# Kernel tuning notes

Hardware: AMD Instinct MI355X
Metric: run time of the kernel (lower is better)

Reference implementation:

```python
import jax, jax.numpy as jnp
import numpy as np

EPS_AGG = 1e-6  # torch code adds 1e-6 to scatter weight sums
EPS_BN = 1e-5


def _pix_idx(loc_orig, H, W):
    # map normalized coords in [-1,1] to flat pixel index on an HxW grid
    loc = jnp.clip(loc_orig, -1.0, 1.0) * 0.5 + 0.5
    ix = jnp.round(loc[..., 0] * (W - 1)).astype(jnp.int32)
    iy = jnp.round(loc[..., 1] * (H - 1)).astype(jnp.int32)
    return iy * W + ix  # [B, N0]


def token2map(x, loc_orig, idx_agg, H, W):
    # scatter token features to a dense map, averaging collisions
    B, N, C = x.shape
    N0 = idx_agg.shape[1]
    idx_hw = _pix_idx(loc_orig, H, W)                                   # [B, N0]
    tok = jnp.take_along_axis(x, idx_agg[..., None], axis=1)            # [B, N0, C]
    flat = (idx_hw + jnp.arange(B, dtype=jnp.int32)[:, None] * (H * W)).reshape(-1)
    sums = jax.ops.segment_sum(tok.reshape(-1, C), flat, num_segments=B * H * W)
    cnt = jax.ops.segment_sum(jnp.ones((B * N0,), x.dtype), flat, num_segments=B * H * W)
    out = sums / (cnt[:, None] + EPS_AGG)
    return out.reshape(B, H, W, C).transpose(0, 3, 1, 2)                # [B, C, H, W]


def map2token(fmap, Nt, loc_orig, idx_agg_t, agg_weight_t):
    # gather map pixels back to Nt target tokens, weighted-averaging per token
    B, C, H, W = fmap.shape
    idx_hw = _pix_idx(loc_orig, H, W)                                   # [B, N0]
    pix = fmap.transpose(0, 2, 3, 1).reshape(B, H * W, C)
    gath = jnp.take_along_axis(pix, idx_hw[..., None], axis=1)          # [B, N0, C]
    flat = (idx_agg_t + jnp.arange(B, dtype=jnp.int32)[:, None] * Nt).reshape(-1)
    num = jax.ops.segment_sum((gath * agg_weight_t[..., None]).reshape(-1, C), flat, num_segments=B * Nt)
    den = jax.ops.segment_sum(agg_weight_t.reshape(-1), flat, num_segments=B * Nt)
    return (num / (den[:, None] + EPS_AGG)).reshape(B, Nt, C)


def token_downup(x, idx_agg_s, idx_agg_t, agg_weight_t, Nt):
    # weighted aggregation from N source tokens to Nt target tokens via N0 original positions
    B, N, C = x.shape
    src = jnp.take_along_axis(x, idx_agg_s[..., None], axis=1)          # [B, N0, C]
    flat = (idx_agg_t + jnp.arange(B, dtype=jnp.int32)[:, None] * Nt).reshape(-1)
    num = jax.ops.segment_sum((src * agg_weight_t[..., None]).reshape(-1, C), flat, num_segments=B * Nt)
    den = jax.ops.segment_sum(agg_weight_t.reshape(-1), flat, num_segments=B * Nt)
    return (num / (den[:, None] + EPS_AGG)).reshape(B, Nt, C)


def batchnorm(x, gamma, beta):
    # BatchNorm2d on [B,C,Nt,1] == per-channel stats over (B, Nt); x here is [B, Nt, C]
    mu = x.mean(axis=(0, 1), keepdims=True)
    var = x.var(axis=(0, 1), keepdims=True)
    return (x - mu) * jax.lax.rsqrt(var + EPS_BN) * gamma + beta


def setup_inputs() -> dict:
    key = jax.random.key(0)
    ks = jax.random.split(key, 12)
    B, N, N0, Nt, Cin, Cout, H, W = 32, 1568, 3136, 784, 256, 512, 56, 56
    x = jax.random.normal(ks[0], (B, N, Cin), dtype=jnp.float32)
    loc_orig = jax.random.uniform(ks[1], (B, N0, 2), dtype=jnp.float32, minval=-1.0, maxval=1.0)
    idx_agg = jax.random.randint(ks[2], (B, N0), 0, N, dtype=jnp.int32)
    agg_weight = jax.random.uniform(ks[3], (B, N0), dtype=jnp.float32)
    idx_agg_t = jax.random.randint(ks[4], (B, N0), 0, Nt, dtype=jnp.int32)
    agg_weight_t = jax.random.uniform(ks[5], (B, N0), dtype=jnp.float32)
    dw_w = jax.random.normal(ks[6], (Cin, 1, 3, 3), dtype=jnp.float32) * 0.1     # depthwise 3x3
    skip_w = jax.random.normal(ks[7], (Cin,), dtype=jnp.float32) * 0.1           # depthwise 1x1
    conv_w = jax.random.normal(ks[8], (Cout, Cin), dtype=jnp.float32) * (1.0 / np.sqrt(Cin))
    gamma1 = jnp.ones((Cin,), jnp.float32); beta1 = jnp.zeros((Cin,), jnp.float32)
    gamma2 = jnp.ones((Cout,), jnp.float32); beta2 = jnp.zeros((Cout,), jnp.float32)
    return {"x": x, "loc_orig": loc_orig, "idx_agg": idx_agg, "agg_weight": agg_weight,
            "idx_agg_t": idx_agg_t, "agg_weight_t": agg_weight_t, "H": H, "W": W, "Nt": Nt,
            "dw_w": dw_w, "skip_w": skip_w, "conv_w": conv_w,
            "gamma1": gamma1, "beta1": beta1, "gamma2": gamma2, "beta2": beta2}


def reference(x, loc_orig, idx_agg, agg_weight, idx_agg_t, agg_weight_t, H, W, Nt,
              dw_w, skip_w, conv_w, gamma1, beta1, gamma2, beta2):
    # token -> map scatter
    x_map = token2map(x, loc_orig, idx_agg, H, W)                       # [B, Cin, H, W]
    # 3x3 depthwise conv, stride 2, padding 1
    Cin = x_map.shape[1]
    x_map = jax.lax.conv_general_dilated(
        x_map, dw_w, window_strides=(2, 2), padding=((1, 1), (1, 1)),
        feature_group_count=Cin, dimension_numbers=("NCHW", "OIHW", "NCHW"))    # [B, Cin, H/2, W/2]
    # map -> target tokens gather
    x_back = map2token(x_map, Nt, loc_orig, idx_agg_t, agg_weight_t)    # [B, Nt, Cin]
    # skip path: token downsample + 1x1 depthwise (per-channel scale)
    xs = token_downup(x, idx_agg, idx_agg_t, agg_weight_t, Nt)          # [B, Nt, Cin]
    xs = xs * skip_w                                                    # dw_skip, groups=Cin, k=1
    y = xs + x_back
    y = batchnorm(y, gamma1, beta1)
    y = jnp.einsum("bnc,oc->bno", y, conv_w)                            # 1x1 conv Cin->Cout
    y = batchnorm(y, gamma2, beta2)
    return jax.nn.relu(y)                                               # [B, Nt, Cout]
```

## Files before the change

kernel.cpp:

```cpp
#include <hip/hip_runtime.h>

constexpr int B    = 32;
constexpr int N    = 1568;
constexpr int N0   = 3136;
constexpr int Nt   = 784;
constexpr int Cin  = 256;
constexpr int Cout = 512;
constexpr int H    = 56;
constexpr int W    = 56;
constexpr int HW   = 3136;
constexpr int Ho   = 28;
constexpr int Wo   = 28;
constexpr int HWo  = 784;
constexpr int RR   = B * Nt;
constexpr int NE   = B * N0;
constexpr int NBP  = B * HW;
constexpr int NBT  = B * Nt;
constexpr int NB   = NBP + NBT;
constexpr int NCHUNK = NB / 256;

constexpr size_t W_HIST  = 0;
constexpr size_t W_S1SUM = NB;
constexpr size_t W_S1SQ  = W_S1SUM + Cin;
constexpr size_t W_S2SUM = W_S1SQ + Cin;
constexpr size_t W_S2SQ  = W_S2SUM + Cout;
constexpr size_t W_OFF   = NB + 1536;
constexpr size_t W_CUR   = W_OFF + NB + 8;
constexpr size_t W_P56   = W_CUR + NB;
constexpr size_t W_P28   = W_P56 + NE;
constexpr size_t W_BSUM  = W_P28 + NE;
constexpr size_t W_SRTS  = W_BSUM + 512;
constexpr size_t W_STS   = W_SRTS + NE;
constexpr size_t W_STP   = W_STS + NE;
constexpr size_t W_STW   = W_STP + NE;
constexpr size_t W_CONVB = W_STW + NE;
constexpr size_t W_YBF   = W_CONVB + (size_t)B * HWo * Cin / 2;
constexpr size_t W_WFB   = W_YBF + (size_t)RR * Cin / 2;
constexpr size_t W_BIAS  = W_WFB + (size_t)Cout * Cin / 2;
constexpr size_t W_A2    = W_BIAS + Cout;
constexpr size_t W_C2    = W_A2 + Cout;
constexpr size_t W_ZB    = W_C2 + Cout;

__device__ __forceinline__ int pix_of(float t, float scale) {
    t = fminf(fmaxf(t, -1.0f), 1.0f);
    float u = __fadd_rn(__fmul_rn(t, 0.5f), 0.5f);
    return (int)rintf(__fmul_rn(u, scale));
}
__device__ __forceinline__ unsigned short f2bf(float f) {
    unsigned int u = __float_as_uint(f);
    u = (u + 0x7fffu + ((u >> 16) & 1u)) >> 16;
    return (unsigned short)u;
}
__device__ __forceinline__ float bf2f(unsigned short h) {
    return __uint_as_float(((unsigned int)h) << 16);
}

__global__ void k_hist(const float* __restrict__ loc, const int* __restrict__ idxt,
                       int* __restrict__ hist, int* __restrict__ p56a, int* __restrict__ p28a) {
    int i = blockIdx.x * 256 + threadIdx.x;
    if (i >= NE) return;
    int b = i / N0;
    float lx = loc[(size_t)2 * i], ly = loc[(size_t)2 * i + 1];
    int p56 = pix_of(ly, 55.0f) * W + pix_of(lx, 55.0f);
    int p28 = pix_of(ly, 27.0f) * Wo + pix_of(lx, 27.0f);
    p56a[i] = p56; p28a[i] = p28;
    atomicAdd(&hist[b * HW + p56], 1);
    atomicAdd(&hist[NBP + b * Nt + idxt[i]], 1);
}

__global__ void k_scanA(const int* __restrict__ hist, int* __restrict__ bsum) {
    __shared__ int sm[256];
    int i = blockIdx.x * 256 + threadIdx.x;
    sm[threadIdx.x] = hist[i];
    __syncthreads();
    for (int d = 128; d > 0; d >>= 1) {
        if (threadIdx.x < d) sm[threadIdx.x] += sm[threadIdx.x + d];
        __syncthreads();
    }
    if (threadIdx.x == 0) bsum[blockIdx.x] = sm[0];
}

__global__ void k_scanB(int* __restrict__ bsum) {
    __shared__ int sm[512];
    int t = threadIdx.x;
    int v = (t < NCHUNK) ? bsum[t] : 0;
    sm[t] = v; __syncthreads();
    for (int d = 1; d < 512; d <<= 1) {
        int u = (t >= d) ? sm[t - d] : 0;
        __syncthreads();
        sm[t] += u;
        __syncthreads();
    }
    if (t < NCHUNK) bsum[t] = sm[t] - v;
}

__global__ void k_scanC(const int* __restrict__ hist, const int* __restrict__ bsum,
                        int* __restrict__ off, int* __restrict__ cur) {
    __shared__ int sm[256];
    int t = threadIdx.x;
    int i = blockIdx.x * 256 + t;
    int v = hist[i];
    sm[t] = v; __syncthreads();
    for (int d = 1; d < 256; d <<= 1) {
        int u = (t >= d) ? sm[t - d] : 0;
        __syncthreads();
        sm[t] += u;
        __syncthreads();
    }
    int excl = bsum[blockIdx.x] + sm[t] - v;
    off[i] = excl; cur[i] = excl;
    if (i == NB - 1) off[NB] = excl + v;
}

__global__ void k_scatteridx(const int* __restrict__ p56a, const int* __restrict__ p28a,
                             const int* __restrict__ idxa, const int* __restrict__ idxt,
                             const float* __restrict__ wt, int* __restrict__ cur,
                             int* __restrict__ srtS, int* __restrict__ sTs,
                             int* __restrict__ sTp, float* __restrict__ sTw) {
    int i = blockIdx.x * 256 + threadIdx.x;
    if (i >= NE) return;
    int b = i / N0;
    int s = idxa[i];
    int posP = atomicAdd(&cur[b * HW + p56a[i]], 1);
    srtS[posP] = s;
    int posT = atomicAdd(&cur[NBP + b * Nt + idxt[i]], 1) - NE;
    sTs[posT] = s; sTp[posT] = p28a[i]; sTw[posT] = wt[i];
}

constexpr int GCAP = 512;
__global__ __launch_bounds__(256) void k_gconv(const float* __restrict__ x,
        const int* __restrict__ off, const int* __restrict__ srtS,
        const float* __restrict__ dww, unsigned short* __restrict__ convb) {
    __shared__ int   sPk[GCAP];
    __shared__ float sRc[GCAP];
    __shared__ int sSt[9], sCt[9], sPref[10];
    int blk = blockIdx.x;
    int c   = threadIdx.x;
    int b   = blk / HWo;
    int rem = blk - b * HWo;
    int oy  = rem / Wo;
    int ox  = rem - oy * Wo;
    if (c < 9) {
        int ky = c / 3, kx = c - ky * 3;
        int iy = oy * 2 - 1 + ky, ix = ox * 2 - 1 + kx;
        int st = 0, ct = 0;
        if (iy >= 0 && iy < H && ix >= 0 && ix < W) {
            int bin = b * HW + iy * W + ix;
            st = off[bin];
            ct = off[bin + 1] - st;
        }
        sSt[c] = st; sCt[c] = ct;
    }
    __syncthreads();
    if (c == 0) {
        int a = 0;
#pragma unroll
        for (int k = 0; k < 9; ++k) { sPref[k] = a; a += sCt[k]; }
        sPref[9] = a;
    }
    __syncthreads();
    int T = sPref[9];
    float wv[9];
#pragma unroll
    for (int k = 0; k < 9; ++k) wv[k] = dww[c * 9 + k];
    float acc = 0.0f;
    for (int base = 0; base < T; base += GCAP) {
        if (c < 9) {
            int ct = sCt[c], pr = sPref[c], st = sSt[c];
            float rc = 1.0f / ((float)ct + 1e-6f);
            int j0 = max(base - pr, 0);
            int j1 = min(base + GCAP - pr, ct);
            for (int j = j0; j < j1; ++j) {
                sPk[pr + j - base] = srtS[st + j] | (c << 16);
                sRc[pr + j - base] = rc;
            }
        }
        __syncthreads();
        int cnt = min(T - base, GCAP);
        for (int j = 0; j < cnt; ++j) {
            int pk = sPk[j];
            float rc = sRc[j];
            int s = pk & 0xFFFF, tap = pk >> 16;
            acc = fmaf(x[((size_t)b * N + s) * Cin + c] * rc, wv[tap], acc);
        }
        __syncthreads();
    }
    convb[(size_t)blk * Cin + c] = f2bf(acc);
}

constexpr int TCAP = 256;
__global__ __launch_bounds__(256) void k_gtok(const float* __restrict__ x,
        const unsigned short* __restrict__ convb, const int* __restrict__ off,
        const int* __restrict__ sTs, const int* __restrict__ sTp,
        const float* __restrict__ sTw, const float* __restrict__ skipw,
        unsigned short* __restrict__ ybf) {
    __shared__ int sS[TCAP];
    __shared__ int sP[TCAP];
    __shared__ float sW[TCAP];
    int bt = blockIdx.x;
    int c  = threadIdx.x;
    int b  = bt / Nt;
    int st = off[NBP + bt] - NE, en = off[NBP + bt + 1] - NE;
    int T = en - st;
    float sk = skipw[c];
    float acc = 0.0f, wsum = 0.0f;
    for (int base = 0; base < T; base += TCAP) {
        int cnt = min(T - base, TCAP);
        if (c < cnt) {
            sS[c] = sTs[st + base + c];
            sP[c] = sTp[st + base + c];
            sW[c] = sTw[st + base + c];
        }
        __syncthreads();
        for (int j = 0; j < cnt; ++j) {
            int s = sS[j], p = sP[j];
            float w = sW[j];
            wsum += w;
            float cv = bf2f(convb[((size_t)b * HWo + p) * Cin + c]);
            acc = fmaf(w, cv + sk * x[((size_t)b * N + s) * Cin + c], acc);
        }
        __syncthreads();
    }
    ybf[(size_t)bt * Cin + c] = f2bf(acc * (1.0f / (wsum + 1e-6f)));
}

__global__ void k_ystats(const unsigned short* __restrict__ ybf,
                         float* __restrict__ s1, float* __restrict__ s1q) {
    int c = threadIdx.x;
    float sum = 0.0f, sq = 0.0f;
    for (int r = blockIdx.x; r < RR; r += gridDim.x) {
        float v = bf2f(ybf[(size_t)r * Cin + c]);
        sum += v;
        sq = fmaf(v, v, sq);
    }
    atomicAdd(&s1[c], sum);
    atomicAdd(&s1q[c], sq);
}

__global__ void k_fold(const float* __restrict__ s1, const float* __restrict__ s1q,
                       const float* __restrict__ g1, const float* __restrict__ b1,
                       const float* __restrict__ convw, unsigned short* __restrict__ wfb,
                       float* __restrict__ bias) {
    int o = blockIdx.x, c = threadIdx.x;
    const float inv = 1.0f / (float)RR;
    float mu  = s1[c] * inv;
    float var = s1q[c] * inv - mu * mu;
    float a   = g1[c] / sqrtf(var + 1e-5f);
    float bs  = b1[c] - mu * a;
    float wv  = convw[(size_t)o * Cin + c];
    wfb[(size_t)o * Cin + c] = f2bf(wv * a);
    __shared__ float red[256];
    red[c] = wv * bs;
    __syncthreads();
    for (int st = 128; st > 0; st >>= 1) {
        if (c < st) red[c] += red[c + st];
        __syncthreads();
    }
    if (c == 0) bias[o] = red[0];
}

typedef __attribute__((ext_vector_type(8))) short short8;
typedef __attribute__((ext_vector_type(4))) float f32x4;

__global__ __launch_bounds__(256) void k_gemm(const unsigned short* __restrict__ A,
        const unsigned short* __restrict__ Bt, const float* __restrict__ bias,
        unsigned short* __restrict__ zb, float* __restrict__ s2, float* __restrict__ s2q) {
    constexpr int BK = 32, LS = 48;
    __shared__ unsigned short As[128 * LS];
    __shared__ unsigned short Bs[128 * LS];
    __shared__ float rsum[128], rsq[128];
    int m0 = blockIdx.x * 128, n0 = blockIdx.y * 128;
    int t = threadIdx.x;
    int wave = t >> 6, lane = t & 63;
    int wm = wave >> 1, wn = wave & 1;
    int l16 = lane & 15, lq = lane >> 4;
    f32x4 acc[4][4];
#pragma unroll
    for (int i = 0; i < 4; ++i)
#pragma unroll
        for (int j = 0; j < 4; ++j) acc[i][j] = (f32x4)0.0f;
    if (t < 128) { rsum[t] = 0.0f; rsq[t] = 0.0f; }

    for (int k0 = 0; k0 < Cin; k0 += BK) {
#pragma unroll
        for (int r2 = 0; r2 < 2; ++r2) {
            int e = r2 * 256 + t;
            int row = e >> 2, kc = (e & 3) * 8;
            *(float4*)&As[row * LS + kc] = *(const float4*)&A[((size_t)(m0 + row)) * Cin + k0 + kc];
            *(float4*)&Bs[row * LS + kc] = *(const float4*)&Bt[((size_t)(n0 + row)) * Cin + k0 + kc];
        }
        __syncthreads();
        short8 af[4], bf[4];
#pragma unroll
        for (int i = 0; i < 4; ++i) {
            af[i] = *(short8*)&As[(wm * 64 + i * 16 + l16) * LS + lq * 8];
            bf[i] = *(short8*)&Bs[(wn * 64 + i * 16 + l16) * LS + lq * 8];
        }
#pragma unroll
        for (int i = 0; i < 4; ++i)
#pragma unroll
            for (int j = 0; j < 4; ++j)
                acc[i][j] = __builtin_amdgcn_mfma_f32_16x16x32_bf16(af[i], bf[j], acc[i][j], 0, 0, 0);
        __syncthreads();
    }
#pragma unroll
    for (int j = 0; j < 4; ++j) {
        int cl  = wn * 64 + j * 16 + l16;
        int col = n0 + cl;
        float bv = bias[col];
        float ps = 0.0f, pq = 0.0f;
#pragma unroll
        for (int i = 0; i < 4; ++i) {
            int rbase = m0 + wm * 64 + i * 16 + lq * 4;
#pragma unroll
            for (int r = 0; r < 4; ++r) {
                float v = acc[i][j][r] + bv;
                zb[(size_t)(rbase + r) * Cout + col] = f2bf(v);
                ps += v;
                pq = fmaf(v, v, pq);
            }
        }
        atomicAdd(&rsum[cl], ps);
        atomicAdd(&rsq[cl], pq);
    }
    __syncthreads();
    if (t < 128) {
        atomicAdd(&s2[n0 + t], rsum[t]);
        atomicAdd(&s2q[n0 + t], rsq[t]);
    }
}

__global__ void k_fold2(const float* __restrict__ s2, const float* __restrict__ s2q,
                        const float* __restrict__ g2, const float* __restrict__ b2,
                        float* __restrict__ a2, float* __restrict__ c2) {
    int o = threadIdx.x;
    const float inv = 1.0f / (float)RR;
    float mu  = s2[o] * inv;
    float var = s2q[o] * inv - mu * mu;
    float a   = g2[o] / sqrtf(var + 1e-5f);
    a2[o] = a;
    c2[o] = b2[o] - mu * a;
}

__global__ void k_final(const unsigned short* __restrict__ zb, const float* __restrict__ a2,
                        const float* __restrict__ c2, float* __restrict__ out) {
    size_t j4 = ((size_t)blockIdx.x * 256 + threadIdx.x) * 4;
    int o = (int)(j4 & (Cout - 1));
    uint2 u = *(const uint2*)&zb[j4];
    float e0 = bf2f((unsigned short)(u.x & 0xffffu));
    float e1 = bf2f((unsigned short)(u.x >> 16));
    float e2 = bf2f((unsigned short)(u.y & 0xffffu));
    float e3 = bf2f((unsigned short)(u.y >> 16));
    float4 r;
    r.x = fmaxf(fmaf(e0, a2[o + 0], c2[o + 0]), 0.0f);
    r.y = fmaxf(fmaf(e1, a2[o + 1], c2[o + 1]), 0.0f);
    r.z = fmaxf(fmaf(e2, a2[o + 2], c2[o + 2]), 0.0f);
    r.w = fmaxf(fmaf(e3, a2[o + 3], c2[o + 3]), 0.0f);
    *(float4*)&out[j4] = r;
}

extern "C" void kernel_launch(void* const* d_in, const int* in_sizes, int n_in,
                              void* d_out, int out_size, void* d_ws, size_t ws_size,
                              hipStream_t stream) {
    const float* x     = (const float*)d_in[0];
    const float* loc   = (const float*)d_in[1];
    const int*   idxa  = (const int*)d_in[2];
    const int*   idxt  = (const int*)d_in[4];
    const float* wt    = (const float*)d_in[5];
    const float* dww   = (const float*)d_in[9];
    const float* skipw = (const float*)d_in[10];
    const float* convw = (const float*)d_in[11];
    const float* g1    = (const float*)d_in[12];
    const float* b1    = (const float*)d_in[13];
    const float* g2    = (const float*)d_in[14];
    const float* b2    = (const float*)d_in[15];

    float* ws = (float*)d_ws;
    int*   hist  = (int*)(ws + W_HIST);
    float* s1sum = ws + W_S1SUM;
    float* s1sq  = ws + W_S1SQ;
    float* s2sum = ws + W_S2SUM;
    float* s2sq  = ws + W_S2SQ;
    int*   off   = (int*)(ws + W_OFF);
    int*   cur   = (int*)(ws + W_CUR);
    int*   p56a  = (int*)(ws + W_P56);
    int*   p28a  = (int*)(ws + W_P28);
    int*   bsum  = (int*)(ws + W_BSUM);
    int*   srtS  = (int*)(ws + W_SRTS);
    int*   sTs   = (int*)(ws + W_STS);
    int*   sTp   = (int*)(ws + W_STP);
    float* sTw   = ws + W_STW;
    unsigned short* convb = (unsigned short*)(ws + W_CONVB);
    unsigned short* ybf   = (unsigned short*)(ws + W_YBF);
    unsigned short* wfb   = (unsigned short*)(ws + W_WFB);
    float* bias  = ws + W_BIAS;
    float* a2    = ws + W_A2;
    float* c2    = ws + W_C2;
    unsigned short* zb = (unsigned short*)(ws + W_ZB);
    float* out   = (float*)d_out;

    hipMemsetAsync(hist, 0, (size_t)(NB + 1536) * sizeof(float), stream);

    k_hist<<<NE / 256, 256, 0, stream>>>(loc, idxt, hist, p56a, p28a);
    k_scanA<<<NCHUNK, 256, 0, stream>>>(hist, bsum);
    k_scanB<<<1, 512, 0, stream>>>(bsum);
    k_scanC<<<NCHUNK, 256, 0, stream>>>(hist, bsum, off, cur);
    k_scatteridx<<<NE / 256, 256, 0, stream>>>(p56a, p28a, idxa, idxt, wt, cur, srtS, sTs, sTp, sTw);

    k_gconv<<<B * HWo, 256, 0, stream>>>(x, off, srtS, dww, convb);
    k_gtok<<<NBT, 256, 0, stream>>>(x, convb, off, sTs, sTp, sTw, skipw, ybf);
    k_ystats<<<256, 256, 0, stream>>>(ybf, s1sum, s1sq);
    k_fold<<<Cout, 256, 0, stream>>>(s1sum, s1sq, g1, b1, convw, wfb, bias);

    dim3 gg(RR / 128, Cout / 128);
    k_gemm<<<gg, 256, 0, stream>>>(ybf, wfb, bias, zb, s2sum, s2sq);
    k_fold2<<<1, 512, 0, stream>>>(s2sum, s2sq, g2, b2, a2, c2);
    k_final<<<(int)(((size_t)RR * Cout) / 1024), 256, 0, stream>>>(zb, a2, c2, out);
}
```

Baseline: 302.7 us.

## Bin source entries directly per conv output pixel with precomputed tap and weight

The binning stage now buckets each original position into every stride-2 conv output pixel whose 3x3 window covers it. Each entry stores the source token, tap index and reciprocal collision count, so k_gconv walks one contiguous list with no per-block 9-bin prefix gathering, shared staging or extra syncs. Token lists are packed into int2 entries and the gather loops are unrolled to keep several loads in flight. In exchange, k_hist and k_scat do up to four atomics and writes per entry, and the conv list is up to four times larger.

```diff
diff --git a/kernel.cpp b/kernel.cpp
--- a/kernel.cpp
+++ b/kernel.cpp
@@ -16,24 +16,23 @@
 constexpr int NE   = B * N0;
 constexpr int NBP  = B * HW;
 constexpr int NBT  = B * Nt;
-constexpr int NB   = NBP + NBT;
-constexpr int NCHUNK = NB / 256;
-
-constexpr size_t W_HIST  = 0;
-constexpr size_t W_S1SUM = NB;
+constexpr int NBO  = B * HWo;
+constexpr int SB   = NBT + NBO;
+constexpr int NCHUNK = SB / 256;
+
+constexpr size_t W_HISTP = 0;
+constexpr size_t W_HISTS = NBP;
+constexpr size_t W_S1SUM = NBP + SB;
 constexpr size_t W_S1SQ  = W_S1SUM + Cin;
 constexpr size_t W_S2SUM = W_S1SQ + Cin;
 constexpr size_t W_S2SQ  = W_S2SUM + Cout;
-constexpr size_t W_OFF   = NB + 1536;
-constexpr size_t W_CUR   = W_OFF + NB + 8;
-constexpr size_t W_P56   = W_CUR + NB;
-constexpr size_t W_P28   = W_P56 + NE;
-constexpr size_t W_BSUM  = W_P28 + NE;
-constexpr size_t W_SRTS  = W_BSUM + 512;
-constexpr size_t W_STS   = W_SRTS + NE;
-constexpr size_t W_STP   = W_STS + NE;
-constexpr size_t W_STW   = W_STP + NE;
-constexpr size_t W_CONVB = W_STW + NE;
+constexpr size_t W_OFF   = NBP + SB + 1536;
+constexpr size_t W_CUR   = W_OFF + SB + 8;
+constexpr size_t W_PC    = W_CUR + SB;
+constexpr size_t W_BSUM  = W_PC + NE;
+constexpr size_t W_LT    = W_BSUM + 512;
+constexpr size_t W_LC    = W_LT + (size_t)2 * NE;
+constexpr size_t W_CONVB = W_LC + (size_t)8 * NE;
 constexpr size_t W_YBF   = W_CONVB + (size_t)B * HWo * Cin / 2;
 constexpr size_t W_WFB   = W_YBF + (size_t)RR * Cin / 2;
 constexpr size_t W_BIAS  = W_WFB + (size_t)Cout * Cin / 2;
@@ -56,16 +55,23 @@
 }
 
 __global__ void k_hist(const float* __restrict__ loc, const int* __restrict__ idxt,
-                       int* __restrict__ hist, int* __restrict__ p56a, int* __restrict__ p28a) {
+                       int* __restrict__ histP, int* __restrict__ histS,
+                       int* __restrict__ pc) {
     int i = blockIdx.x * 256 + threadIdx.x;
     if (i >= NE) return;
     int b = i / N0;
     float lx = loc[(size_t)2 * i], ly = loc[(size_t)2 * i + 1];
-    int p56 = pix_of(ly, 55.0f) * W + pix_of(lx, 55.0f);
-    int p28 = pix_of(ly, 27.0f) * Wo + pix_of(lx, 27.0f);
-    p56a[i] = p56; p28a[i] = p28;
-    atomicAdd(&hist[b * HW + p56], 1);
-    atomicAdd(&hist[NBP + b * Nt + idxt[i]], 1);
+    int ix = pix_of(lx, 55.0f), iy = pix_of(ly, 55.0f);
+    int jx = pix_of(lx, 27.0f), jy = pix_of(ly, 27.0f);
+    int p56 = iy * W + ix, p28 = jy * Wo + jx;
+    pc[i] = p56 | (p28 << 16);
+    atomicAdd(&histP[b * HW + p56], 1);
+    atomicAdd(&histS[b * Nt + idxt[i]], 1);
+    int oy_lo = iy >> 1, oy_hi = min(Ho - 1, (iy + 1) >> 1);
+    int ox_lo = ix >> 1, ox_hi = min(Wo - 1, (ix + 1) >> 1);
+    for (int oy = oy_lo; oy <= oy_hi; ++oy)
+        for (int ox = ox_lo; ox <= ox_hi; ++ox)
+            atomicAdd(&histS[NBT + b * HWo + oy * Wo + ox], 1);
 }
 
 __global__ void k_scanA(const int* __restrict__ hist, int* __restrict__ bsum) {
@@ -109,117 +115,95 @@
     }
     int excl = bsum[blockIdx.x] + sm[t] - v;
     off[i] = excl; cur[i] = excl;
-    if (i == NB - 1) off[NB] = excl + v;
-}
-
-__global__ void k_scatteridx(const int* __restrict__ p56a, const int* __restrict__ p28a,
-                             const int* __restrict__ idxa, const int* __restrict__ idxt,
-                             const float* __restrict__ wt, int* __restrict__ cur,
-                             int* __restrict__ srtS, int* __restrict__ sTs,
-                             int* __restrict__ sTp, float* __restrict__ sTw) {
+    if (i == SB - 1) off[SB] = excl + v;
+}
+
+__global__ void k_scat(const int* __restrict__ pc, const int* __restrict__ idxa,
+                       const int* __restrict__ idxt, const float* __restrict__ wt,
+                       const int* __restrict__ histP, int* __restrict__ cur,
+                       int2* __restrict__ listT, int2* __restrict__ listC) {
     int i = blockIdx.x * 256 + threadIdx.x;
     if (i >= NE) return;
     int b = i / N0;
+    int v = pc[i];
+    int p56 = v & 0xFFFF, p28 = v >> 16;
     int s = idxa[i];
-    int posP = atomicAdd(&cur[b * HW + p56a[i]], 1);
-    srtS[posP] = s;
-    int posT = atomicAdd(&cur[NBP + b * Nt + idxt[i]], 1) - NE;
-    sTs[posT] = s; sTp[posT] = p28a[i]; sTw[posT] = wt[i];
-}
-
-constexpr int GCAP = 512;
+    int posT = atomicAdd(&cur[b * Nt + idxt[i]], 1);
+    listT[posT] = make_int2(s | (p28 << 16), __float_as_int(wt[i]));
+    float wrc = 1.0f / ((float)histP[b * HW + p56] + 1e-6f);
+    int wrci = __float_as_int(wrc);
+    int iy = p56 / W, ix = p56 - iy * W;
+    int oy_lo = iy >> 1, oy_hi = min(Ho - 1, (iy + 1) >> 1);
+    int ox_lo = ix >> 1, ox_hi = min(Wo - 1, (ix + 1) >> 1);
+    for (int oy = oy_lo; oy <= oy_hi; ++oy)
+        for (int ox = ox_lo; ox <= ox_hi; ++ox) {
+            int tap = (iy - (2 * oy - 1)) * 3 + (ix - (2 * ox - 1));
+            int posC = atomicAdd(&cur[NBT + b * HWo + oy * Wo + ox], 1) - NE;
+            listC[posC] = make_int2(s | (tap << 16), wrci);
+        }
+}
+
 __global__ __launch_bounds__(256) void k_gconv(const float* __restrict__ x,
-        const int* __restrict__ off, const int* __restrict__ srtS,
+        const int* __restrict__ off, const int2* __restrict__ listC,
         const float* __restrict__ dww, unsigned short* __restrict__ convb) {
-    __shared__ int   sPk[GCAP];
-    __shared__ float sRc[GCAP];
-    __shared__ int sSt[9], sCt[9], sPref[10];
-    int blk = blockIdx.x;
-    int c   = threadIdx.x;
-    int b   = blk / HWo;
-    int rem = blk - b * HWo;
-    int oy  = rem / Wo;
-    int ox  = rem - oy * Wo;
-    if (c < 9) {
-        int ky = c / 3, kx = c - ky * 3;
-        int iy = oy * 2 - 1 + ky, ix = ox * 2 - 1 + kx;
-        int st = 0, ct = 0;
-        if (iy >= 0 && iy < H && ix >= 0 && ix < W) {
-            int bin = b * HW + iy * W + ix;
-            st = off[bin];
-            ct = off[bin + 1] - st;
-        }
-        sSt[c] = st; sCt[c] = ct;
-    }
+    __shared__ float wsm[9 * 256];
+    int blk = blockIdx.x, c = threadIdx.x;
+    int b = blk / HWo;
+#pragma unroll
+    for (int k = 0; k < 9; ++k) wsm[k * 256 + c] = dww[c * 9 + k];
+    int st = off[NBT + blk] - NE, en = off[NBT + blk + 1] - NE;
     __syncthreads();
-    if (c == 0) {
-        int a = 0;
-#pragma unroll
-        for (int k = 0; k < 9; ++k) { sPref[k] = a; a += sCt[k]; }
-        sPref[9] = a;
-    }
-    __syncthreads();
-    int T = sPref[9];
-    float wv[9];
-#pragma unroll
-    for (int k = 0; k < 9; ++k) wv[k] = dww[c * 9 + k];
+    const float* xb = x + (size_t)b * N * Cin + c;
     float acc = 0.0f;
-    for (int base = 0; base < T; base += GCAP) {
-        if (c < 9) {
-            int ct = sCt[c], pr = sPref[c], st = sSt[c];
-            float rc = 1.0f / ((float)ct + 1e-6f);
-            int j0 = max(base - pr, 0);
-            int j1 = min(base + GCAP - pr, ct);
-            for (int j = j0; j < j1; ++j) {
-                sPk[pr + j - base] = srtS[st + j] | (c << 16);
-                sRc[pr + j - base] = rc;
-            }
-        }
-        __syncthreads();
-        int cnt = min(T - base, GCAP);
-        for (int j = 0; j < cnt; ++j) {
-            int pk = sPk[j];
-            float rc = sRc[j];
-            int s = pk & 0xFFFF, tap = pk >> 16;
-            acc = fmaf(x[((size_t)b * N + s) * Cin + c] * rc, wv[tap], acc);
-        }
-        __syncthreads();
+    int j = st;
+    for (; j + 4 <= en; j += 4) {
+        int2 e0 = listC[j], e1 = listC[j + 1], e2 = listC[j + 2], e3 = listC[j + 3];
+        float v0 = xb[(size_t)(e0.x & 0xFFFF) * Cin];
+        float v1 = xb[(size_t)(e1.x & 0xFFFF) * Cin];
+        float v2 = xb[(size_t)(e2.x & 0xFFFF) * Cin];
+        float v3 = xb[(size_t)(e3.x & 0xFFFF) * Cin];
+        acc = fmaf(v0 * __int_as_float(e0.y), wsm[(e0.x >> 16) * 256 + c], acc);
+        acc = fmaf(v1 * __int_as_float(e1.y), wsm[(e1.x >> 16) * 256 + c], acc);
+        acc = fmaf(v2 * __int_as_float(e2.y), wsm[(e2.x >> 16) * 256 + c], acc);
+        acc = fmaf(v3 * __int_as_float(e3.y), wsm[(e3.x >> 16) * 256 + c], acc);
+    }
+    for (; j < en; ++j) {
+        int2 e = listC[j];
+        acc = fmaf(xb[(size_t)(e.x & 0xFFFF) * Cin] * __int_as_float(e.y),
+                   wsm[(e.x >> 16) * 256 + c], acc);
     }
     convb[(size_t)blk * Cin + c] = f2bf(acc);
 }
 
-constexpr int TCAP = 256;
 __global__ __launch_bounds__(256) void k_gtok(const float* __restrict__ x,
         const unsigned short* __restrict__ convb, const int* __restrict__ off,
-        const int* __restrict__ sTs, const int* __restrict__ sTp,
-        const float* __restrict__ sTw, const float* __restrict__ skipw,
+        const int2* __restrict__ listT, const float* __restrict__ skipw,
         unsigned short* __restrict__ ybf) {
-    __shared__ int sS[TCAP];
-    __shared__ int sP[TCAP];
-    __shared__ float sW[TCAP];
-    int bt = blockIdx.x;
-    int c  = threadIdx.x;
-    int b  = bt / Nt;
-    int st = off[NBP + bt] - NE, en = off[NBP + bt + 1] - NE;
-    int T = en - st;
+    int bt = blockIdx.x, c = threadIdx.x;
+    int b = bt / Nt;
+    int st = off[bt], en = off[bt + 1];
     float sk = skipw[c];
+    const float* xb = x + (size_t)b * N * Cin + c;
+    const unsigned short* cb = convb + (size_t)b * HWo * Cin + c;
     float acc = 0.0f, wsum = 0.0f;
-    for (int base = 0; base < T; base += TCAP) {
-        int cnt = min(T - base, TCAP);
-        if (c < cnt) {
-            sS[c] = sTs[st + base + c];
-            sP[c] = sTp[st + base + c];
-            sW[c] = sTw[st + base + c];
-        }
-        __syncthreads();
-        for (int j = 0; j < cnt; ++j) {
-            int s = sS[j], p = sP[j];
-            float w = sW[j];
-            wsum += w;
-            float cv = bf2f(convb[((size_t)b * HWo + p) * Cin + c]);
-            acc = fmaf(w, cv + sk * x[((size_t)b * N + s) * Cin + c], acc);
-        }
-        __syncthreads();
+    int j = st;
+    for (; j + 2 <= en; j += 2) {
+        int2 e0 = listT[j], e1 = listT[j + 1];
+        float w0 = __int_as_float(e0.y), w1 = __int_as_float(e1.y);
+        float cv0 = bf2f(cb[(size_t)(e0.x >> 16) * Cin]);
+        float cv1 = bf2f(cb[(size_t)(e1.x >> 16) * Cin]);
+        float xv0 = xb[(size_t)(e0.x & 0xFFFF) * Cin];
+        float xv1 = xb[(size_t)(e1.x & 0xFFFF) * Cin];
+        wsum += w0 + w1;
+        acc = fmaf(w0, cv0 + sk * xv0, acc);
+        acc = fmaf(w1, cv1 + sk * xv1, acc);
+    }
+    for (; j < en; ++j) {
+        int2 e = listT[j];
+        float w = __int_as_float(e.y);
+        wsum += w;
+        float cv = bf2f(cb[(size_t)(e.x >> 16) * Cin]);
+        acc = fmaf(w, cv + sk * xb[(size_t)(e.x & 0xFFFF) * Cin], acc);
     }
     ybf[(size_t)bt * Cin + c] = f2bf(acc * (1.0f / (wsum + 1e-6f)));
 }
@@ -376,20 +360,18 @@
     const float* b2    = (const float*)d_in[15];
 
     float* ws = (float*)d_ws;
-    int*   hist  = (int*)(ws + W_HIST);
+    int*   histP = (int*)(ws + W_HISTP);
+    int*   histS = (int*)(ws + W_HISTS);
     float* s1sum = ws + W_S1SUM;
     float* s1sq  = ws + W_S1SQ;
     float* s2sum = ws + W_S2SUM;
     float* s2sq  = ws + W_S2SQ;
     int*   off   = (int*)(ws + W_OFF);
     int*   cur   = (int*)(ws + W_CUR);
-    int*   p56a  = (int*)(ws + W_P56);
-    int*   p28a  = (int*)(ws + W_P28);
+    int*   pc    = (int*)(ws + W_PC);
     int*   bsum  = (int*)(ws + W_BSUM);
-    int*   srtS  = (int*)(ws + W_SRTS);
-    int*   sTs   = (int*)(ws + W_STS);
-    int*   sTp   = (int*)(ws + W_STP);
-    float* sTw   = ws + W_STW;
+    int2*  listT = (int2*)(ws + W_LT);
+    int2*  listC = (int2*)(ws + W_LC);
     unsigned short* convb = (unsigned short*)(ws + W_CONVB);
     unsigned short* ybf   = (unsigned short*)(ws + W_YBF);
     unsigned short* wfb   = (unsigned short*)(ws + W_WFB);
@@ -399,16 +381,16 @@
     unsigned short* zb = (unsigned short*)(ws + W_ZB);
     float* out   = (float*)d_out;
 
-    hipMemsetAsync(hist, 0, (size_t)(NB + 1536) * sizeof(float), stream);
-
-    k_hist<<<NE / 256, 256, 0, stream>>>(loc, idxt, hist, p56a, p28a);
-    k_scanA<<<NCHUNK, 256, 0, stream>>>(hist, bsum);
+    hipMemsetAsync(histP, 0, (size_t)(NBP + SB + 1536) * sizeof(float), stream);
+
+    k_hist<<<NE / 256, 256, 0, stream>>>(loc, idxt, histP, histS, pc);
+    k_scanA<<<NCHUNK, 256, 0, stream>>>(histS, bsum);
     k_scanB<<<1, 512, 0, stream>>>(bsum);
-    k_scanC<<<NCHUNK, 256, 0, stream>>>(hist, bsum, off, cur);
-    k_scatteridx<<<NE / 256, 256, 0, stream>>>(p56a, p28a, idxa, idxt, wt, cur, srtS, sTs, sTp, sTw);
-
-    k_gconv<<<B * HWo, 256, 0, stream>>>(x, off, srtS, dww, convb);
-    k_gtok<<<NBT, 256, 0, stream>>>(x, convb, off, sTs, sTp, sTw, skipw, ybf);
+    k_scanC<<<NCHUNK, 256, 0, stream>>>(histS, bsum, off, cur);
+    k_scat<<<NE / 256, 256, 0, stream>>>(pc, idxa, idxt, wt, histP, cur, listT, listC);
+
+    k_gconv<<<NBO, 256, 0, stream>>>(x, off, listC, dww, convb);
+    k_gtok<<<NBT, 256, 0, stream>>>(x, convb, off, listT, skipw, ybf);
     k_ystats<<<256, 256, 0, stream>>>(ybf, s1sum, s1sq);
     k_fold<<<Cout, 256, 0, stream>>>(s1sum, s1sq, g1, b1, convw, wfb, bias);
 
```

Result: no change. 300.7 us (-0.7%).
